# Kernel optimization log

Measured on AMD Instinct MI355X. Metric: run time of the kernel, lower is better.

Reference implementation:

```python
import jax, jax.numpy as jnp
import numpy as np

B, N_ENC, N_DEC = 32, 512, 512
IN_V, OUT_V = 2000, 2000
H, F, K, P = 256, 256, 5, 4  # P = |G| (indices < P are masked to 0 before embedding)
E_ENC, E_DEC = 128, 128


def setup_inputs() -> dict:
    key = jax.random.key(0)
    ks = jax.random.split(key, 16)
    s = lambda i, shape, scale=0.05: jax.random.normal(ks[i], shape, jnp.float32) * scale
    return dict(
        xs_idx=jax.random.randint(ks[0], (B, N_ENC), 0, IN_V),
        ys_idx=jax.random.randint(ks[1], (B, N_DEC), 0, OUT_V),
        gembed_W=s(2, (IN_V, F)),
        gconv_W=s(3, (K, F, F)),
        gdecode_W=s(4, (F, OUT_V)),
        enc_embed=s(5, (IN_V, E_ENC)),
        dec_embed=s(6, (OUT_V, E_DEC)),
        enc_Wih=s(7, (4 * H, E_ENC)),
        enc_Whh=s(8, (4 * H, H)),
        enc_b=jnp.zeros((4 * H,), jnp.float32),
        dec_Wih=s(9, (4 * H, E_DEC)),
        dec_Whh=s(10, (4 * H, H)),
        dec_b=jnp.zeros((4 * H,), jnp.float32),
        T=jax.random.uniform(ks[11], (H, 2 * H), jnp.float32, -0.5, 0.5),
    )


def _lstm(x, Wih, Whh, b, h0, c0):
    # x: (B, T, D); PyTorch gate order i, f, g, o
    def step(carry, xt):
        h, c = carry
        z = xt @ Wih.T + h @ Whh.T + b
        i, f, g, o = jnp.split(z, 4, axis=-1)
        c = jax.nn.sigmoid(f) * c + jax.nn.sigmoid(i) * jnp.tanh(g)
        h = jax.nn.sigmoid(o) * jnp.tanh(c)
        return (h, c), h
    (hT, cT), hs = jax.lax.scan(step, (h0, c0), jnp.swapaxes(x, 0, 1))
    return jnp.swapaxes(hs, 0, 1), hT, cT


def reference(xs_idx, ys_idx, gembed_W, gconv_W, gdecode_W, enc_embed, dec_embed,
              enc_Wih, enc_Whh, enc_b, dec_Wih, dec_Whh, dec_b, T):
    # --- G-equivariant stack: per-encoder-position distribution over output vocab ---
    e = jnp.tanh(gembed_W[xs_idx])  # (B, Ne, F)
    c = jax.lax.conv_general_dilated(e, gconv_W, (1,), 'SAME',
                                     dimension_numbers=('NWC', 'WIO', 'NWC'))
    probs = jax.nn.softmax(jnp.tanh(c) @ gdecode_W, axis=-1)  # (B, Ne, V)
    # encoder_scores[b, i, j] = probs[b, i, ys[b, j]]
    idx = jnp.broadcast_to(ys_idx[:, None, :], (probs.shape[0], probs.shape[1], ys_idx.shape[1]))
    encoder_scores = jnp.take_along_axis(probs, idx, axis=2)  # (B, Ne, Nd)

    # --- invariant LSTM encoder (indices < |G| masked to 0) ---
    xm = jnp.where(xs_idx < P, 0, xs_idx)
    x_embed = enc_embed[xm]  # (B, Ne, E)
    z = jnp.zeros((x_embed.shape[0], H), jnp.float32)
    henc, hT, cT = _lstm(x_embed, enc_Wih, enc_Whh, enc_b, z, z)
    hback, _, _ = _lstm(jnp.flip(x_embed, axis=1), enc_Wih, enc_Whh, enc_b, z, z)
    hback = jnp.flip(hback, axis=1)

    # --- decoder LSTM, initialized with encoder final state ---
    ym = jnp.where(ys_idx < P, 0, ys_idx)
    y_embed = dec_embed[ym]
    out, _, _ = _lstm(y_embed, dec_Wih, dec_Whh, dec_b, hT, cT)
    h_dec = jnp.concatenate([henc[:, -1:, :], out], axis=1)[:, :-1, :]  # (B, Nd, H)
    h_enc = jnp.concatenate([henc, hback], axis=2)  # (B, Ne, 2H)

    # --- bilinear alignment scores: eij[b, i, j] = h_dec[b, j] . (T @ h_enc[b, i]) ---
    Th = jnp.einsum('he,bie->bih', T, h_enc)           # (B, Ne, H)
    eij = jnp.einsum('bjh,bih->bij', h_dec, Th)        # (B, Ne, Nd)
    align = jax.nn.softmax(eij, axis=1)                # softmax over encoder positions

    p = jnp.sum(jnp.log(jnp.sum(encoder_scores * align, axis=1)), axis=1)  # (B,)
    return -jnp.sum(p)
```

## Files before the change

kernel.cpp:

```cpp
#include <hip/hip_runtime.h>

typedef _Float16 f16;
typedef _Float16 f16x2 __attribute__((ext_vector_type(2)));
typedef _Float16 f16x4 __attribute__((ext_vector_type(4)));
typedef _Float16 f16x8 __attribute__((ext_vector_type(8)));
typedef float    f32x4 __attribute__((ext_vector_type(4)));
typedef int      i32x4 __attribute__((ext_vector_type(4)));
typedef unsigned int u32;
typedef unsigned short u16;

#define DEVI static __device__ __forceinline__

static constexpr int LDT = 40;
static constexpr int LDA = 264;

DEVI float sigf(float x){ return 1.f/(1.f + __expf(-x)); }
DEVI float tanh_c(float x){
  x = fminf(fmaxf(x, -15.f), 15.f);
  float e = __expf(2.f*x);
  return (e - 1.f)/(e + 1.f);
}
DEVI float sig_f(float x){ return __builtin_amdgcn_rcpf(1.f + __expf(-x)); }
DEVI float tanh_f(float x){ return 1.f - 2.f*__builtin_amdgcn_rcpf(1.f + __expf(2.f*x)); }
DEVI float wmax16(float v){
  #pragma unroll
  for (int m=1;m<16;m<<=1) v = fmaxf(v, __shfl_xor(v, m, 64));
  return v;
}
DEVI float wsum16(float v){
  #pragma unroll
  for (int m=1;m<16;m<<=1) v += __shfl_xor(v, m, 64);
  return v;
}
DEVI f16x8 frag_ld(const f16* p){ return *(const f16x8*)p; }
DEVI void stage_tileh(int t256, const f16* src, int ld, f16* dst){
  int row = t256>>2, qq = t256&3;
  *(f16x8*)(dst + row*LDT + qq*8) = *(const f16x8*)(src + (size_t)row*ld + qq*8);
}
#define ZERO4(acc) { f32x4 _z = {0.f,0.f,0.f,0.f}; acc[0]=_z; acc[1]=_z; acc[2]=_z; acc[3]=_z; }

DEVI void gemm64h(int t256, const f16* A, int lda, const f16* Bm, int ldb, int K,
                  f16* lA, f16* lB, f32x4 acc[4]){
  const int lane = t256 & 63, wv = t256 >> 6;
  const int l15 = lane & 15, kq = lane >> 4;
  for (int k0=0; k0<K; k0+=32){
    __syncthreads();
    stage_tileh(t256, A + k0, lda, lA);
    stage_tileh(t256, Bm + k0, ldb, lB);
    __syncthreads();
    f16x8 af = frag_ld(lA + (16*wv + l15)*LDT + kq*8);
    #pragma unroll
    for (int nt=0; nt<4; nt++){
      f16x8 bf = frag_ld(lB + (16*nt + l15)*LDT + kq*8);
      acc[nt] = __builtin_amdgcn_mfma_f32_16x16x32_f16(af, bf, acc[nt], 0,0,0);
    }
  }
}

__global__ void k_cvt(const float* __restrict__ s, f16* __restrict__ d, int n){
  int i = blockIdx.x*256 + threadIdx.x;
  if (i < n) d[i] = (f16)s[i];
}
__global__ void k_gconvT(const float* __restrict__ s, f16* __restrict__ d){
  int id = blockIdx.x;
  int fo = threadIdx.x;
  d[(size_t)fo*1280 + id] = (f16)s[(size_t)id*256 + fo];
}
__global__ void k_gdecT(const float* __restrict__ s, f16* __restrict__ d){
  int v = blockIdx.x, f = threadIdx.x;
  f16 val = (f16)0.f;
  if (v < 2000) val = (f16)s[(size_t)f*2000 + v];
  d[(size_t)v*256 + f] = val;
}
__global__ void k_epad(const int* __restrict__ xs, const float* __restrict__ gemb, f16* __restrict__ epad){
  int id = blockIdx.x;
  int f = threadIdx.x;
  int b = id / 516, p = id % 516;
  float v = 0.f;
  if (p >= 2 && p < 514){ int idx = xs[b*512 + p - 2]; v = tanh_c(gemb[(size_t)idx*256 + f]); }
  epad[(size_t)id*256 + f] = (f16)v;
}
__global__ void k_embx(const int* __restrict__ xs, const int* __restrict__ ys,
                       const float* __restrict__ eemb, const float* __restrict__ demb,
                       f16* __restrict__ xo, f16* __restrict__ yo){
  int id = blockIdx.x; int f = threadIdx.x;
  bool dec = id >= 32*512; int id2 = dec ? id - 32*512 : id;
  int idx = dec ? ys[id2] : xs[id2];
  if (idx < 4) idx = 0;
  const float* src = (dec ? demb : eemb) + (size_t)idx*128;
  (dec ? yo : xo)[(size_t)id2*128 + f] = (f16)src[f];
}

__global__ void k_wmax(const float* __restrict__ Whh, u32* __restrict__ ws){
  int i = (blockIdx.x*256 + threadIdx.x)*4;
  float m = 0.f;
  #pragma unroll
  for (int j=0;j<4;j++) m = fmaxf(m, fabsf(Whh[i+j]));
  #pragma unroll
  for (int d=1; d<64; d<<=1) m = fmaxf(m, __shfl_xor(m, d, 64));
  if ((threadIdx.x & 63) == 0) atomicMax(ws, __float_as_uint(m));
}
__global__ void k_wq8(const float* __restrict__ Whh, const u32* __restrict__ ws,
                      i32x4* __restrict__ Wq){
  const int bid = blockIdx.x;
  const int l = threadIdx.x;
  const int kt = bid & 3, t8 = (bid >> 2) & 7, w = bid >> 5;
  const int r15 = l & 15;
  const int u4 = r15 >> 2, g = r15 & 3;
  const int unit = w*32 + t8*4 + u4;
  const int row = g*256 + unit;
  const int k0  = kt*64 + (l >> 4)*16;
  const float scale = 127.f / __uint_as_float(ws[0]);
  int dw[4];
  #pragma unroll
  for (int d=0; d<4; d++){
    u32 acc = 0;
    #pragma unroll
    for (int j=0; j<4; j++){
      float q = __builtin_rintf(Whh[(size_t)row*256 + k0 + d*4 + j] * scale);
      int qi = (int)fminf(fmaxf(q, -127.f), 127.f);
      acc |= ((u32)qi & 0xffu) << (8*j);
    }
    dw[d] = (int)acc;
  }
  i32x4 v = { dw[0], dw[1], dw[2], dw[3] };
  Wq[(size_t)bid*64 + l] = v;
}

__global__ __launch_bounds__(256,4) void k_conv(const f16* __restrict__ epad, const f16* __restrict__ gcT, f16* __restrict__ tf){
  __shared__ f16 lA[64*LDT], lB[64*LDT];
  const int m0 = blockIdx.x*64, n0 = blockIdx.y*64;
  const int b = m0 >> 9, n = m0 & 511;
  f32x4 acc[4]; ZERO4(acc);
  gemm64h(threadIdx.x, epad + ((size_t)b*516 + n)*256, 256, gcT + (size_t)n0*1280, 1280, 1280, lA, lB, acc);
  const int lane=threadIdx.x&63, wv=threadIdx.x>>6, l15=lane&15, kq=lane>>4;
  #pragma unroll
  for (int nt=0;nt<4;nt++)
    #pragma unroll
    for (int r=0;r<4;r++)
      tf[(size_t)(m0 + 16*wv + 4*kq + r)*256 + n0 + nt*16 + l15] = (f16)tanh_c(acc[nt][r]);
}

DEVI void ku_body(int t256, int m0, int n0, const f16* X, const f16* Wih,
                  const float* bias, f16* U, f16* lA, f16* lB){
  f32x4 acc[4]; ZERO4(acc);
  gemm64h(t256, X + (size_t)m0*128, 128, Wih + (size_t)n0*128, 128, 128, lA, lB, acc);
  const int lane=t256&63, wv=t256>>6, l15=lane&15, kq=lane>>4;
  #pragma unroll
  for (int nt=0;nt<4;nt++){
    int n = n0 + nt*16 + l15;
    float bv = bias[n];
    int cnew = (n & 255)*4 + (n >> 8);
    #pragma unroll
    for (int r=0;r<4;r++)
      U[(size_t)(m0 + 16*wv + 4*kq + r)*1024 + cnew] = (f16)(acc[nt][r] + bv);
  }
}

__global__ __launch_bounds__(256,4) void k_u(const f16* __restrict__ X, const f16* __restrict__ Wih,
                                             const float* __restrict__ bias, f16* __restrict__ U){
  __shared__ f16 lA[64*LDT], lB[64*LDT];
  ku_body(threadIdx.x, blockIdx.x*64, blockIdx.y*64, X, Wih, bias, U, lA, lB);
}

DEVI void th_body(int t256, int m0, int n0, const f16* henh, const f16* Tf, f16* Th,
                  f16* lA, f16* lB){
  f32x4 acc[4]; ZERO4(acc);
  gemm64h(t256, henh + (size_t)m0*512, 512, Tf + (size_t)n0*512, 512, 512, lA, lB, acc);
  const int lane=t256&63, wv=t256>>6, l15=lane&15, kq=lane>>4;
  #pragma unroll
  for (int nt=0;nt<4;nt++)
    #pragma unroll
    for (int r=0;r<4;r++)
      Th[(size_t)(m0 + 16*wv + 4*kq + r)*256 + n0 + nt*16 + l15] = (f16)acc[nt][r];
}

DEVI void pass1_body(int tid, int mt, int ns, const f16* tf, const f16* gdT,
                     float* mxp, float* sep, f16* lA, f16* lB2, float* mxs2, float* ses2){
  const int half = tid >> 8, t256 = tid & 255;
  const int lane = tid & 63, wv = t256 >> 6, l15 = lane & 15, kq = lane >> 4;
  f16* lB = lB2 + half*(64*LDT);
  {
    const f16* A = tf + (size_t)mt*64*256;
    int row = tid >> 3, c8 = tid & 7;
    #pragma unroll
    for (int q=0;q<4;q++)
      *(f16x8*)(lA + row*LDA + c8*32 + q*8) = *(const f16x8*)(A + (size_t)row*256 + c8*32 + q*8);
  }
  if (t256 < 64){ mxs2[half*64 + t256] = -1e30f; ses2[half*64 + t256] = 0.f; }
  __syncthreads();
  for (int nci=0; nci<4; nci++){
    const int nc = half*4 + nci;
    const int nbase = ns*512 + nc*64;
    const f16* Bm = gdT + (size_t)nbase*256;
    f32x4 acc[4]; ZERO4(acc);
    for (int k0=0; k0<256; k0+=32){
      __syncthreads();
      stage_tileh(t256, Bm + k0, 256, lB);
      __syncthreads();
      f16x8 af = frag_ld(lA + (16*wv + l15)*LDA + k0 + kq*8);
      #pragma unroll
      for (int nt=0; nt<4; nt++){
        f16x8 bf = frag_ld(lB + (16*nt + l15)*LDT + kq*8);
        acc[nt] = __builtin_amdgcn_mfma_f32_16x16x32_f16(af, bf, acc[nt], 0,0,0);
      }
    }
    #pragma unroll
    for (int r=0;r<4;r++){
      float av[4]; float cm = -1e30f;
      #pragma unroll
      for (int nt=0;nt<4;nt++){
        int gcol = nbase + nt*16 + l15;
        float a = (gcol < 2000) ? acc[nt][r] : -1e30f;
        av[nt] = a; cm = fmaxf(cm, a);
      }
      cm = wmax16(cm);
      int rr = half*64 + 16*wv + 4*kq + r;
      float old = mxs2[rr];
      float nm = fmaxf(old, cm);
      float ss = 0.f;
      #pragma unroll
      for (int nt=0;nt<4;nt++) ss += __expf(av[nt] - nm);
      ss = wsum16(ss);
      if (l15 == 0){
        ses2[rr] = ses2[rr]*__expf(old - nm) + ss;
        mxs2[rr] = nm;
      }
    }
  }
  __syncthreads();
  if (tid < 64){
    float m0 = mxs2[tid], m1 = mxs2[64+tid];
    float nm = fmaxf(m0, m1);
    float se = ses2[tid]*__expf(m0-nm) + ses2[64+tid]*__expf(m1-nm);
    mxp[(size_t)ns*16384 + mt*64 + tid] = nm;
    sep[(size_t)ns*16384 + mt*64 + tid] = se;
  }
}

__global__ void k_comb1(const float* __restrict__ mxp, const float* __restrict__ sep,
                        float* __restrict__ mx, float* __restrict__ se){
  int m = blockIdx.x*256 + threadIdx.x;
  float best = -1e30f;
  #pragma unroll
  for (int k=0;k<4;k++) best = fmaxf(best, mxp[(size_t)k*16384 + m]);
  float s = 0.f;
  #pragma unroll
  for (int k=0;k<4;k++) s += sep[(size_t)k*16384 + m] * __expf(mxp[(size_t)k*16384 + m] - best);
  mx[m] = best; se[m] = s;
}

DEVI void pass2_body(int t256, int it, int jt, int b, const f16* tf, const f16* gdT,
                     const int* ys, const float* mx, const float* se, f16* scT,
                     f16* lA, f16* lB, int* jv){
  const int lane=t256&63, wv=t256>>6, l15=lane&15, kq=lane>>4;
  if (t256<64) jv[t256] = ys[b*512 + jt*64 + t256];
  const f16* A = tf + ((size_t)b*512 + it*64)*256;
  f32x4 acc[4]; ZERO4(acc);
  for (int k0=0;k0<256;k0+=32){
    __syncthreads();
    stage_tileh(t256, A + k0, 256, lA);
    { int row=t256>>2, qq=t256&3;
      *(f16x8*)(lB + row*LDT + qq*8) = *(const f16x8*)(gdT + (size_t)jv[row]*256 + k0 + qq*8); }
    __syncthreads();
    f16x8 af = frag_ld(lA + (16*wv+l15)*LDT + kq*8);
    #pragma unroll
    for (int nt=0;nt<4;nt++){
      f16x8 bf = frag_ld(lB + (16*nt+l15)*LDT + kq*8);
      acc[nt] = __builtin_amdgcn_mfma_f32_16x16x32_f16(af, bf, acc[nt], 0,0,0);
    }
  }
  float mxv[4], rsev[4];
  #pragma unroll
  for (int r=0;r<4;r++){
    int i_ = it*64 + 16*wv + 4*kq + r;
    mxv[r] = mx[b*512 + i_];
    rsev[r] = 1.f / se[b*512 + i_];
  }
  #pragma unroll
  for (int nt=0;nt<4;nt++){
    int j_ = jt*64 + nt*16 + l15;
    #pragma unroll
    for (int r=0;r<4;r++){
      int i_ = it*64 + 16*wv + 4*kq + r;
      scT[((size_t)b*512 + j_)*512 + i_] = (f16)(__expf(acc[nt][r] - mxv[r]) * rsev[r]);
    }
  }
}

__global__ __launch_bounds__(256,2) void k_final(const f16* __restrict__ hdec, const f16* __restrict__ Th,
                                                 const f16* __restrict__ scT,
                                                 float* __restrict__ pmx, float* __restrict__ pden, float* __restrict__ pnum){
  __shared__ f16 lA[64*LDA];
  __shared__ f16 lB[64*LDT];
  __shared__ float mx_s[64], den_s[64], num_s[64];
  const int is = blockIdx.x, jt = blockIdx.y, b = blockIdx.z;
  const int tid = threadIdx.x, lane=tid&63, wv=tid>>6, l15=lane&15, kq=lane>>4;
  {
    const f16* A = hdec + ((size_t)b*512 + jt*64)*256;
    int row = tid>>2, qq = tid&3;
    #pragma unroll
    for (int c=0;c<8;c++)
      *(f16x8*)(lA + row*LDA + c*32 + qq*8) = *(const f16x8*)(A + (size_t)row*256 + c*32 + qq*8);
  }
  if (tid<64){ mx_s[tid]=-1e30f; den_s[tid]=0.f; num_s[tid]=0.f; }
  __syncthreads();
  for (int ic=0; ic<4; ic++){
    const int i0 = is*256 + ic*64;
    const f16* Bm = Th + ((size_t)b*512 + i0)*256;
    f32x4 acc[4]; ZERO4(acc);
    for (int k0=0;k0<256;k0+=32){
      __syncthreads();
      stage_tileh(tid, Bm + k0, 256, lB);
      __syncthreads();
      f16x8 af = frag_ld(lA + (16*wv+l15)*LDA + k0 + kq*8);
      #pragma unroll
      for (int nt=0;nt<4;nt++){
        f16x8 bf = frag_ld(lB + (16*nt+l15)*LDT + kq*8);
        acc[nt] = __builtin_amdgcn_mfma_f32_16x16x32_f16(af, bf, acc[nt], 0,0,0);
      }
    }
    #pragma unroll
    for (int r=0;r<4;r++){
      int jl = 16*wv + 4*kq + r;
      float av[4]; float cm=-1e30f;
      #pragma unroll
      for (int nt=0;nt<4;nt++){ av[nt]=acc[nt][r]; cm=fmaxf(cm,av[nt]); }
      cm = wmax16(cm);
      float old = mx_s[jl], nm = fmaxf(old, cm);
      float ds=0.f, nsum=0.f;
      const size_t srow = ((size_t)b*512 + jt*64 + jl)*512;
      #pragma unroll
      for (int nt=0;nt<4;nt++){
        float e = __expf(av[nt]-nm);
        float sc = (float)scT[srow + i0 + nt*16 + l15];
        ds += e; nsum += sc*e;
      }
      ds = wsum16(ds); nsum = wsum16(nsum);
      if (l15==0){
        float fac = __expf(old-nm);
        den_s[jl] = den_s[jl]*fac + ds;
        num_s[jl] = num_s[jl]*fac + nsum;
        mx_s[jl] = nm;
      }
    }
  }
  __syncthreads();
  if (tid<64){
    size_t idx = (((size_t)b*512) + jt*64 + tid)*2 + is;
    pmx[idx]=mx_s[tid]; pden[idx]=den_s[tid]; pnum[idx]=num_s[tid];
  }
}

__global__ void k_comb2(const float* __restrict__ pmx, const float* __restrict__ pden,
                        const float* __restrict__ pnum, float* __restrict__ out){
  const int b = blockIdx.x, j = threadIdx.x;
  size_t base = ((size_t)b*512 + j)*2;
  float m0=pmx[base], m1=pmx[base+1];
  float m = fmaxf(m0,m1);
  float e0=__expf(m0-m), e1=__expf(m1-m);
  float den = pden[base]*e0 + pden[base+1]*e1;
  float num = pnum[base]*e0 + pnum[base+1]*e1;
  float lp = __logf(num) - __logf(den);
  __shared__ float red[512];
  red[j] = lp;
  __syncthreads();
  for (int st=256; st>0; st>>=1){ if (j<st) red[j]+=red[j+st]; __syncthreads(); }
  if (j==0) atomicAdd(out, -red[0]);
}

DEVI void lstm_core(char* smem, const f16* U, const i32x4* Wq, const u32* ws,
                    u16* hout, float* hTcT, u16* hdec0, int nsteps, int mode, int bid)
{
  char* h8b = smem;
  const int tid = threadIdx.x;
  const int lane = tid & 63, w = tid >> 6;
  const int l15 = lane & 15, kq = lane >> 4;
  const int s = l15 & 3, p = l15 >> 2;
  const int uA = w*32 + 4*p + kq;
  const int uB = uA + 16;

  int dir = 0, b0;
  if (mode == 0){ dir = bid >> 3; b0 = (bid & 7)*4; }
  else b0 = bid*4;

  const float zscale = __uint_as_float(ws[0]) * (1.f/(127.f*127.f));

  i32x4 aw[32];
  #pragma unroll
  for (int f=0; f<32; f++) aw[f] = Wq[(size_t)(w*32 + f)*64 + lane];

  float cA = 0.f, cB = 0.f;
  if (mode == 0){
    ((u32*)h8b)[tid] = 0u;
  } else {
    const float* hp = hTcT + (size_t)(b0+s)*512;
    float hA = hp[uA], hB = hp[uB];
    cA = hp[256 + uA]; cB = hp[256 + uB];
    h8b[((uA>>4)*4 + s)*16 + (uA&15)] = (char)(int)__builtin_rintf(hA*127.f);
    h8b[((uB>>4)*4 + s)*16 + (uB&15)] = (char)(int)__builtin_rintf(hB*127.f);
  }

  const f16* Urow = U + (size_t)(b0+s)*512*1024;
  f16x4 uvA, uvB;
  {
    int tp0 = dir ? (nsteps-1) : 0;
    uvA = *(const f16x4*)(Urow + (size_t)tp0*1024 + uA*4);
    uvB = *(const f16x4*)(Urow + (size_t)tp0*1024 + uB*4);
  }
  __syncthreads();

  int cur = 0;
  #pragma unroll 1
  for (int t=0; t<nsteps; ++t){
    const int tpos = dir ? (nsteps-1-t) : t;
    int tn = dir ? (nsteps-2-t >= 0 ? nsteps-2-t : 0) : (t+1 < nsteps ? t+1 : nsteps-1);
    f16x4 puA = *(const f16x4*)(Urow + (size_t)tn*1024 + uA*4);
    f16x4 puB = *(const f16x4*)(Urow + (size_t)tn*1024 + uB*4);

    const char* hc = h8b + cur*1024;
    i32x4 bf[4];
    #pragma unroll
    for (int kt=0; kt<4; kt++)
      bf[kt] = *(const i32x4*)(hc + ((kt*4 + kq)*4 + s)*16);

    const int nxt = cur ^ 1;
    char* hn = h8b + nxt*1024;

    i32x4 acc0[4];
    #pragma unroll
    for (int t8=0; t8<4; t8++){
      i32x4 d = {0,0,0,0};
      #pragma unroll
      for (int kt=0; kt<4; kt++)
        d = __builtin_amdgcn_mfma_i32_16x16x64_i8(aw[t8*4+kt], bf[kt], d, 0,0,0);
      acc0[t8] = d;
    }

    i32x4 vA;
    #pragma unroll
    for (int e=0; e<4; e++){
      int x01 = (p&1) ? acc0[1][e] : acc0[0][e];
      int x23 = (p&1) ? acc0[3][e] : acc0[2][e];
      vA[e] = (p&2) ? x23 : x01;
    }
    float hA_;
    {
      float z0 = fmaf((float)vA[0], zscale, (float)uvA[0]);
      float z1 = fmaf((float)vA[1], zscale, (float)uvA[1]);
      float z2 = fmaf((float)vA[2], zscale, (float)uvA[2]);
      float z3 = fmaf((float)vA[3], zscale, (float)uvA[3]);
      cA = sig_f(z1)*cA + sig_f(z0)*tanh_f(z2);
      hA_ = sig_f(z3)*tanh_f(cA);
    }
    hn[((uA>>4)*4 + s)*16 + (uA&15)] = (char)(int)__builtin_rintf(hA_*127.f);

    i32x4 acc1[4];
    #pragma unroll
    for (int t8=0; t8<4; t8++){
      i32x4 d = {0,0,0,0};
      #pragma unroll
      for (int kt=0; kt<4; kt++)
        d = __builtin_amdgcn_mfma_i32_16x16x64_i8(aw[(t8+4)*4+kt], bf[kt], d, 0,0,0);
      acc1[t8] = d;
    }

    i32x4 vB;
    #pragma unroll
    for (int e=0; e<4; e++){
      int y01 = (p&1) ? acc1[1][e] : acc1[0][e];
      int y23 = (p&1) ? acc1[3][e] : acc1[2][e];
      vB[e] = (p&2) ? y23 : y01;
    }
    float hB_;
    {
      float z0 = fmaf((float)vB[0], zscale, (float)uvB[0]);
      float z1 = fmaf((float)vB[1], zscale, (float)uvB[1]);
      float z2 = fmaf((float)vB[2], zscale, (float)uvB[2]);
      float z3 = fmaf((float)vB[3], zscale, (float)uvB[3]);
      cB = sig_f(z1)*cB + sig_f(z0)*tanh_f(z2);
      hB_ = sig_f(z3)*tanh_f(cB);
    }
    hn[((uB>>4)*4 + s)*16 + (uB&15)] = (char)(int)__builtin_rintf(hB_*127.f);

    f16 fA = (f16)hA_, fB = (f16)hB_;
    if (mode == 0){
      u16* hr = hout + ((size_t)(b0+s)*512 + tpos)*512 + dir*256;
      hr[uA] = __builtin_bit_cast(u16, fA);
      hr[uB] = __builtin_bit_cast(u16, fB);
      if (!dir && t == nsteps-1){
        hdec0[(size_t)(b0+s)*512*256 + uA] = __builtin_bit_cast(u16, fA);
        hdec0[(size_t)(b0+s)*512*256 + uB] = __builtin_bit_cast(u16, fB);
        float* hp = hTcT + (size_t)(b0+s)*512;
        hp[uA] = hA_; hp[uB] = hB_;
        hp[256+uA] = cA; hp[256+uB] = cB;
      }
    } else {
      u16* hr = hout + ((size_t)(b0+s)*512 + (t+1))*256;
      hr[uA] = __builtin_bit_cast(u16, fA);
      hr[uB] = __builtin_bit_cast(u16, fB);
    }

    asm volatile("s_waitcnt lgkmcnt(0)" ::: "memory");
    __builtin_amdgcn_s_barrier();
    asm volatile("" ::: "memory");
    __builtin_amdgcn_sched_barrier(0);

    cur = nxt;
    uvA = puA; uvB = puB;
  }
}

__global__ __launch_bounds__(512,2) void k_mega_enc(
    const f16* __restrict__ Uenc, const i32x4* __restrict__ Wqe, const u32* __restrict__ wse,
    u16* __restrict__ henh, float* __restrict__ hTcT, u16* __restrict__ hdec0,
    const f16* __restrict__ tf, const f16* __restrict__ gdT,
    float* __restrict__ mxp, float* __restrict__ sep,
    const f16* __restrict__ yemb, const f16* __restrict__ Wihd,
    const float* __restrict__ db, f16* __restrict__ Udec)
{
  __shared__ __align__(16) char smem[45056];
  const int bid = blockIdx.x;
  const int tid = threadIdx.x;
  if (bid < 16){
    lstm_core(smem, Uenc, Wqe, wse, henh, hTcT, hdec0, 512, 0, bid);
    return;
  }
  if (bid >= 256 && bid < 272) return;
  const int w = (bid < 256) ? (bid - 16) : (bid - 32);
  for (int v = w; v < 3072; v += 480){
    __syncthreads();
    if (v < 1024){
      int mt = v >> 2;
      int ns = v & 3;
      pass1_body(tid, mt, ns, tf, gdT, mxp, sep,
                 (f16*)smem, (f16*)(smem + 33792), (float*)(smem + 44032), (float*)(smem + 44544));
    } else {
      int vb = v - 1024;
      int half = tid >> 8, t256 = tid & 255;
      int vbm = vb >> 4, ny = vb & 15;
      int m0 = (vbm*2 + half)*64;
      int n0 = ny*64;
      char* base = smem + half*10240;
      ku_body(t256, m0, n0, yemb, Wihd, db, Udec, (f16*)base, (f16*)(base + 5120));
    }
  }
}

__global__ __launch_bounds__(512,2) void k_mega_dec(
    const f16* __restrict__ Udec, const i32x4* __restrict__ Wqd, const u32* __restrict__ wsd,
    u16* __restrict__ hdec, float* __restrict__ hTcT,
    const f16* __restrict__ tf, const f16* __restrict__ gdT, const int* __restrict__ ys,
    const float* __restrict__ mx, const float* __restrict__ se, f16* __restrict__ scT,
    const f16* __restrict__ henh, const f16* __restrict__ Tf, f16* __restrict__ Th)
{
  __shared__ __align__(16) char smem[24576];
  const int bid = blockIdx.x;
  const int tid = threadIdx.x;
  if (bid < 8){
    lstm_core(smem, Udec, Wqd, wsd, hdec, hTcT, hdec, 511, 1, bid);
    return;
  }
  if (bid >= 256 && bid < 264) return;
  const int w = (bid < 256) ? (bid - 8) : (bid - 16);
  for (int v = w; v < 1536; v += 496){
    __syncthreads();
    if (v < 1024){
      int half = tid >> 8, t256 = tid & 255;
      int b = v >> 5, rem = v & 31;
      int jt = rem >> 2, it = (rem & 3)*2 + half;
      char* base = smem + half*10496;
      pass2_body(t256, it, jt, b, tf, gdT, ys, mx, se, scT,
                 (f16*)base, (f16*)(base + 5120), (int*)(base + 10240));
    } else {
      int vb = v - 1024;
      int half = tid >> 8, t256 = tid & 255;
      int m0 = ((vb >> 2)*2 + half)*64;
      int n0 = (vb & 3)*64;
      char* base = smem + half*10240;
      th_body(t256, m0, n0, henh, Tf, Th, (f16*)base, (f16*)(base + 5120));
    }
  }
}

extern "C" void kernel_launch(void* const* d_in, const int* in_sizes, int n_in,
                              void* d_out, int out_size, void* d_ws, size_t ws_size,
                              hipStream_t stream)
{
  (void)in_sizes; (void)n_in; (void)out_size;
  const int*   xs    = (const int*)d_in[0];
  const int*   ys    = (const int*)d_in[1];
  const float* gemb  = (const float*)d_in[2];
  const float* gconv = (const float*)d_in[3];
  const float* gdec  = (const float*)d_in[4];
  const float* eemb  = (const float*)d_in[5];
  const float* demb  = (const float*)d_in[6];
  const float* eWih  = (const float*)d_in[7];
  const float* eWhh  = (const float*)d_in[8];
  const float* eb    = (const float*)d_in[9];
  const float* dWih  = (const float*)d_in[10];
  const float* dWhh  = (const float*)d_in[11];
  const float* db    = (const float*)d_in[12];
  const float* Tm    = (const float*)d_in[13];

  char* wsb = (char*)d_ws;
  size_t off = 0;
  auto take = [&](size_t bytes)->char*{ char* p = wsb + off; off += (bytes + 255) & ~(size_t)255; return p; };
  f16* epad  = (f16*)take((size_t)32*516*256*2);
  f16* tf    = (f16*)take((size_t)32*512*256*2);
  f16* xemb  = (f16*)take((size_t)32*512*128*2);
  f16* yemb  = (f16*)take((size_t)32*512*128*2);
  f16* Uenc  = (f16*)take((size_t)32*512*1024*2);
  f16* Udec  = (f16*)take((size_t)32*512*1024*2);
  f16* henh  = (f16*)take((size_t)32*512*512*2);
  f16* hdec  = (f16*)take((size_t)32*512*256*2);
  f16* Th    = (f16*)take((size_t)32*512*256*2);
  f16* scT   = (f16*)take((size_t)32*512*512*2);
  float* mx  = (float*)take((size_t)16384*4);
  float* se  = (float*)take((size_t)16384*4);
  float* mxp = (float*)take((size_t)4*16384*4);
  float* sep = (float*)take((size_t)4*16384*4);
  float* pmx = (float*)take((size_t)32*512*2*4);
  float* pden= (float*)take((size_t)32*512*2*4);
  float* pnum= (float*)take((size_t)32*512*2*4);
  float* hTcT= (float*)take((size_t)32*512*4);
  f16* Wihe  = (f16*)take((size_t)1024*128*2);
  f16* Wihd  = (f16*)take((size_t)1024*128*2);
  f16* Tf    = (f16*)take((size_t)256*512*2);
  f16* gcT   = (f16*)take((size_t)256*1280*2);
  f16* gdT   = (f16*)take((size_t)2048*256*2);
  i32x4* Wq8e = (i32x4*)take((size_t)256*64*16);
  i32x4* Wq8d = (i32x4*)take((size_t)256*64*16);
  u32* wsc   = (u32*)take(8);
  if (off > ws_size) return;

  hipMemsetAsync(d_out, 0, sizeof(float), stream);
  hipMemsetAsync(wsc, 0, 8, stream);

  k_cvt<<<dim3(512),  256, 0, stream>>>(eWih, Wihe, 1024*128);
  k_cvt<<<dim3(512),  256, 0, stream>>>(dWih, Wihd, 1024*128);
  k_cvt<<<dim3(512),  256, 0, stream>>>(Tm,   Tf,   256*512);
  k_gconvT<<<dim3(1280), 256, 0, stream>>>(gconv, gcT);
  k_gdecT <<<dim3(2048), 256, 0, stream>>>(gdec, gdT);
  k_wmax<<<dim3(256), 256, 0, stream>>>(eWhh, wsc + 0);
  k_wmax<<<dim3(256), 256, 0, stream>>>(dWhh, wsc + 1);
  k_wq8<<<dim3(256), 64, 0, stream>>>(eWhh, wsc + 0, Wq8e);
  k_wq8<<<dim3(256), 64, 0, stream>>>(dWhh, wsc + 1, Wq8d);
  k_epad<<<dim3(32*516), 256, 0, stream>>>(xs, gemb, epad);
  k_embx<<<dim3(2*32*512), 128, 0, stream>>>(xs, ys, eemb, demb, xemb, yemb);

  k_conv<<<dim3(256,4), 256, 0, stream>>>(epad, gcT, tf);
  k_u<<<dim3(256,16), 256, 0, stream>>>(xemb, Wihe, eb, Uenc);

  k_mega_enc<<<dim3(512), 512, 0, stream>>>(Uenc, Wq8e, wsc + 0, (u16*)henh, hTcT, (u16*)hdec,
                                            tf, gdT, mxp, sep, yemb, Wihd, db, Udec);
  k_comb1<<<dim3(64), 256, 0, stream>>>(mxp, sep, mx, se);

  k_mega_dec<<<dim3(512), 512, 0, stream>>>(Udec, Wq8d, wsc + 1, (u16*)hdec, hTcT,
                                            tf, gdT, ys, mx, se, scT, henh, Tf, Th);

  k_final<<<dim3(2,8,32), 256, 0, stream>>>(hdec, Th, scT, pmx, pden, pnum);
  k_comb2<<<dim3(32), 512, 0, stream>>>(pmx, pden, pnum, (float*)d_out);
}
```

Before: 1.140 ms.

## Software-pipeline LSTM recurrence across two half-unit groups with staggered gate math

Splits the hidden units into two halves (A: units 0-127, B: 128-255) and reorders the quantized recurrent weights to match. The B-half gate nonlinearities from the previous step are interleaved with the A-half MFMAs of the current step, using explicit sched_barriers and a mid-step barrier so the second half of the K dimension is read after B's h is written. The aim is to hide transcendental and elementwise latency on the serial recurrence critical path behind matrix-core work. The cost is an extra barrier per step, a one-step-delayed B pipeline with an epilogue, and more complex indexing that is easy to get subtly wrong.

```diff
diff --git a/kernel.cpp b/kernel.cpp
--- a/kernel.cpp
+++ b/kernel.cpp
@@ -10,18 +10,16 @@
 typedef unsigned short u16;
 
 #define DEVI static __device__ __forceinline__
+#define SBAR() __builtin_amdgcn_sched_barrier(0)
 
 static constexpr int LDT = 40;
 static constexpr int LDA = 264;
 
-DEVI float sigf(float x){ return 1.f/(1.f + __expf(-x)); }
 DEVI float tanh_c(float x){
   x = fminf(fmaxf(x, -15.f), 15.f);
   float e = __expf(2.f*x);
   return (e - 1.f)/(e + 1.f);
 }
-DEVI float sig_f(float x){ return __builtin_amdgcn_rcpf(1.f + __expf(-x)); }
-DEVI float tanh_f(float x){ return 1.f - 2.f*__builtin_amdgcn_rcpf(1.f + __expf(2.f*x)); }
 DEVI float wmax16(float v){
   #pragma unroll
   for (int m=1;m<16;m<<=1) v = fmaxf(v, __shfl_xor(v, m, 64));
@@ -107,7 +105,7 @@
   const int kt = bid & 3, t8 = (bid >> 2) & 7, w = bid >> 5;
   const int r15 = l & 15;
   const int u4 = r15 >> 2, g = r15 & 3;
-  const int unit = w*32 + t8*4 + u4;
+  const int unit = (t8 < 4) ? (w*16 + t8*4 + u4) : (128 + w*16 + (t8-4)*4 + u4);
   const int row = g*256 + unit;
   const int k0  = kt*64 + (l >> 4)*16;
   const float scale = 127.f / __uint_as_float(ws[0]);
@@ -377,8 +375,9 @@
   const int lane = tid & 63, w = tid >> 6;
   const int l15 = lane & 15, kq = lane >> 4;
   const int s = l15 & 3, p = l15 >> 2;
-  const int uA = w*32 + 4*p + kq;
-  const int uB = uA + 16;
+  const int uA = w*16 + 4*p + kq;
+  const int uB = uA + 128;
+  const int u15 = uA & 15;
 
   int dir = 0, b0;
   if (mode == 0){ dir = bid >> 3; b0 = (bid & 7)*4; }
@@ -391,23 +390,31 @@
   for (int f=0; f<32; f++) aw[f] = Wq[(size_t)(w*32 + f)*64 + lane];
 
   float cA = 0.f, cB = 0.f;
+  f16 fB_init = (f16)0.f;
+  char hB_q0 = 0;
   if (mode == 0){
     ((u32*)h8b)[tid] = 0u;
   } else {
     const float* hp = hTcT + (size_t)(b0+s)*512;
-    float hA = hp[uA], hB = hp[uB];
+    float hA0 = hp[uA], hB0 = hp[uB];
     cA = hp[256 + uA]; cB = hp[256 + uB];
-    h8b[((uA>>4)*4 + s)*16 + (uA&15)] = (char)(int)__builtin_rintf(hA*127.f);
-    h8b[((uB>>4)*4 + s)*16 + (uB&15)] = (char)(int)__builtin_rintf(hB*127.f);
+    h8b[(w*4 + s)*16 + u15]     = (char)(int)__builtin_rintf(hA0*127.f);
+    hB_q0 = (char)(int)__builtin_rintf(hB0*127.f);
+    h8b[((8+w)*4 + s)*16 + u15] = hB_q0;
+    fB_init = (f16)hB0;
   }
 
   const f16* Urow = U + (size_t)(b0+s)*512*1024;
-  f16x4 uvA, uvB;
+  f16x4 uvA, uvB, uvBp;
   {
     int tp0 = dir ? (nsteps-1) : 0;
     uvA = *(const f16x4*)(Urow + (size_t)tp0*1024 + uA*4);
     uvB = *(const f16x4*)(Urow + (size_t)tp0*1024 + uB*4);
   }
+  uvBp = uvB;
+  i32x4 accBp[4];
+  { i32x4 z = {0,0,0,0}; accBp[0]=z; accBp[1]=z; accBp[2]=z; accBp[3]=z; }
+  int tpos_prev = dir ? (nsteps-1) : 0;
   __syncthreads();
 
   int cur = 0;
@@ -418,96 +425,161 @@
     f16x4 puA = *(const f16x4*)(Urow + (size_t)tn*1024 + uA*4);
     f16x4 puB = *(const f16x4*)(Urow + (size_t)tn*1024 + uB*4);
 
-    const char* hc = h8b + cur*1024;
-    i32x4 bf[4];
-    #pragma unroll
-    for (int kt=0; kt<4; kt++)
-      bf[kt] = *(const i32x4*)(hc + ((kt*4 + kq)*4 + s)*16);
-
+    char* bufc = h8b + cur*1024;
     const int nxt = cur ^ 1;
-    char* hn = h8b + nxt*1024;
-
-    i32x4 acc0[4];
-    #pragma unroll
-    for (int t8=0; t8<4; t8++){
-      i32x4 d = {0,0,0,0};
-      #pragma unroll
-      for (int kt=0; kt<4; kt++)
-        d = __builtin_amdgcn_mfma_i32_16x16x64_i8(aw[t8*4+kt], bf[kt], d, 0,0,0);
-      acc0[t8] = d;
-    }
-
-    i32x4 vA;
+    char* bufn = h8b + nxt*1024;
+    const bool live = (t > 0);
+
+    i32x4 bf0 = *(const i32x4*)(bufc + (kq*4 + s)*16);
+    i32x4 bf1 = *(const i32x4*)(bufc + ((4+kq)*4 + s)*16);
+
+    i32x4 accA[4], accB[4];
+    { i32x4 z = {0,0,0,0};
+      accA[0]=z; accA[1]=z; accA[2]=z; accA[3]=z;
+      accB[0]=z; accB[1]=z; accB[2]=z; accB[3]=z; }
+
+    i32x4 vB;
     #pragma unroll
     for (int e=0; e<4; e++){
-      int x01 = (p&1) ? acc0[1][e] : acc0[0][e];
-      int x23 = (p&1) ? acc0[3][e] : acc0[2][e];
-      vA[e] = (p&2) ? x23 : x01;
-    }
-    float hA_;
-    {
-      float z0 = fmaf((float)vA[0], zscale, (float)uvA[0]);
-      float z1 = fmaf((float)vA[1], zscale, (float)uvA[1]);
-      float z2 = fmaf((float)vA[2], zscale, (float)uvA[2]);
-      float z3 = fmaf((float)vA[3], zscale, (float)uvA[3]);
-      cA = sig_f(z1)*cA + sig_f(z0)*tanh_f(z2);
-      hA_ = sig_f(z3)*tanh_f(cA);
-    }
-    hn[((uA>>4)*4 + s)*16 + (uA&15)] = (char)(int)__builtin_rintf(hA_*127.f);
-
-    i32x4 acc1[4];
-    #pragma unroll
-    for (int t8=0; t8<4; t8++){
-      i32x4 d = {0,0,0,0};
-      #pragma unroll
-      for (int kt=0; kt<4; kt++)
-        d = __builtin_amdgcn_mfma_i32_16x16x64_i8(aw[(t8+4)*4+kt], bf[kt], d, 0,0,0);
-      acc1[t8] = d;
-    }
-
-    i32x4 vB;
-    #pragma unroll
-    for (int e=0; e<4; e++){
-      int y01 = (p&1) ? acc1[1][e] : acc1[0][e];
-      int y23 = (p&1) ? acc1[3][e] : acc1[2][e];
-      vB[e] = (p&2) ? y23 : y01;
-    }
-    float hB_;
-    {
-      float z0 = fmaf((float)vB[0], zscale, (float)uvB[0]);
-      float z1 = fmaf((float)vB[1], zscale, (float)uvB[1]);
-      float z2 = fmaf((float)vB[2], zscale, (float)uvB[2]);
-      float z3 = fmaf((float)vB[3], zscale, (float)uvB[3]);
-      cB = sig_f(z1)*cB + sig_f(z0)*tanh_f(z2);
-      hB_ = sig_f(z3)*tanh_f(cB);
-    }
-    hn[((uB>>4)*4 + s)*16 + (uB&15)] = (char)(int)__builtin_rintf(hB_*127.f);
-
-    f16 fA = (f16)hA_, fB = (f16)hB_;
+      int x01 = (p&1) ? accBp[1][e] : accBp[0][e];
+      int x23 = (p&1) ? accBp[3][e] : accBp[2][e];
+      vB[e] = (p&2) ? x23 : x01;
+    }
+    float zb0 = fmaf((float)vB[0], zscale, (float)uvBp[0]);
+    float zb1 = fmaf((float)vB[1], zscale, (float)uvBp[1]);
+    float zb2 = fmaf((float)vB[2], zscale, (float)uvBp[2]);
+    float zb3 = fmaf((float)vB[3], zscale, (float)uvBp[3]);
+    SBAR();
+    #pragma unroll
+    for (int t8=0; t8<4; t8++) accA[t8] = __builtin_amdgcn_mfma_i32_16x16x64_i8(aw[t8*4+0], bf0, accA[t8], 0,0,0);
+    SBAR();
+    float eb0 = __expf(-zb0), eb1 = __expf(-zb1), eb2 = __expf(2.f*zb2), eb3 = __expf(-zb3);
+    SBAR();
+    #pragma unroll
+    for (int t8=0; t8<4; t8++) accB[t8] = __builtin_amdgcn_mfma_i32_16x16x64_i8(aw[(4+t8)*4+0], bf0, accB[t8], 0,0,0);
+    SBAR();
+    float bi = __builtin_amdgcn_rcpf(1.f + eb0);
+    float bfg= __builtin_amdgcn_rcpf(1.f + eb1);
+    float bg = 1.f - 2.f*__builtin_amdgcn_rcpf(1.f + eb2);
+    float bo = __builtin_amdgcn_rcpf(1.f + eb3);
+    SBAR();
+    #pragma unroll
+    for (int t8=0; t8<4; t8++) accA[t8] = __builtin_amdgcn_mfma_i32_16x16x64_i8(aw[t8*4+1], bf1, accA[t8], 0,0,0);
+    SBAR();
+    float cBn = bfg*cB + bi*bg;
+    float ebc = __expf(2.f*cBn);
+    float tB  = 1.f - 2.f*__builtin_amdgcn_rcpf(1.f + ebc);
+    float hB_ = bo*tB;
+    cB = live ? cBn : cB;
+    char hq   = live ? (char)(int)__builtin_rintf(hB_*127.f) : hB_q0;
+    f16 fB    = live ? (f16)hB_ : fB_init;
+    bufc[((8+w)*4 + s)*16 + u15] = hq;
     if (mode == 0){
-      u16* hr = hout + ((size_t)(b0+s)*512 + tpos)*512 + dir*256;
-      hr[uA] = __builtin_bit_cast(u16, fA);
-      hr[uB] = __builtin_bit_cast(u16, fB);
-      if (!dir && t == nsteps-1){
-        hdec0[(size_t)(b0+s)*512*256 + uA] = __builtin_bit_cast(u16, fA);
-        hdec0[(size_t)(b0+s)*512*256 + uB] = __builtin_bit_cast(u16, fB);
-        float* hp = hTcT + (size_t)(b0+s)*512;
-        hp[uA] = hA_; hp[uB] = hB_;
-        hp[256+uA] = cA; hp[256+uB] = cB;
-      }
+      hout[(((size_t)(b0+s)*512 + tpos_prev)*512) + dir*256 + uB] = __builtin_bit_cast(u16, fB);
     } else {
-      u16* hr = hout + ((size_t)(b0+s)*512 + (t+1))*256;
-      hr[uA] = __builtin_bit_cast(u16, fA);
-      hr[uB] = __builtin_bit_cast(u16, fB);
-    }
+      hout[((size_t)(b0+s)*512 + (tpos_prev+1))*256 + uB] = __builtin_bit_cast(u16, fB);
+    }
+    SBAR();
+    #pragma unroll
+    for (int t8=0; t8<4; t8++) accB[t8] = __builtin_amdgcn_mfma_i32_16x16x64_i8(aw[(4+t8)*4+1], bf1, accB[t8], 0,0,0);
 
     asm volatile("s_waitcnt lgkmcnt(0)" ::: "memory");
     __builtin_amdgcn_s_barrier();
     asm volatile("" ::: "memory");
     __builtin_amdgcn_sched_barrier(0);
 
-    cur = nxt;
-    uvA = puA; uvB = puB;
+    i32x4 bf2 = *(const i32x4*)(bufc + ((8+kq)*4 + s)*16);
+    i32x4 bf3 = *(const i32x4*)(bufc + ((12+kq)*4 + s)*16);
+
+    #pragma unroll
+    for (int t8=0; t8<4; t8++) accA[t8] = __builtin_amdgcn_mfma_i32_16x16x64_i8(aw[t8*4+2], bf2, accA[t8], 0,0,0);
+    SBAR();
+    #pragma unroll
+    for (int t8=0; t8<4; t8++) accA[t8] = __builtin_amdgcn_mfma_i32_16x16x64_i8(aw[t8*4+3], bf3, accA[t8], 0,0,0);
+    SBAR();
+    i32x4 vA;
+    #pragma unroll
+    for (int e=0; e<4; e++){
+      int x01 = (p&1) ? accA[1][e] : accA[0][e];
+      int x23 = (p&1) ? accA[3][e] : accA[2][e];
+      vA[e] = (p&2) ? x23 : x01;
+    }
+    float za0 = fmaf((float)vA[0], zscale, (float)uvA[0]);
+    float za1 = fmaf((float)vA[1], zscale, (float)uvA[1]);
+    float za2 = fmaf((float)vA[2], zscale, (float)uvA[2]);
+    float za3 = fmaf((float)vA[3], zscale, (float)uvA[3]);
+    SBAR();
+    #pragma unroll
+    for (int t8=0; t8<4; t8++) accB[t8] = __builtin_amdgcn_mfma_i32_16x16x64_i8(aw[(4+t8)*4+2], bf2, accB[t8], 0,0,0);
+    SBAR();
+    float ea0 = __expf(-za0), ea1 = __expf(-za1), ea2 = __expf(2.f*za2), ea3 = __expf(-za3);
+    SBAR();
+    #pragma unroll
+    for (int t8=0; t8<4; t8++) accB[t8] = __builtin_amdgcn_mfma_i32_16x16x64_i8(aw[(4+t8)*4+3], bf3, accB[t8], 0,0,0);
+    SBAR();
+    float ai = __builtin_amdgcn_rcpf(1.f + ea0);
+    float af = __builtin_amdgcn_rcpf(1.f + ea1);
+    float ag = 1.f - 2.f*__builtin_amdgcn_rcpf(1.f + ea2);
+    float ao = __builtin_amdgcn_rcpf(1.f + ea3);
+    cA = af*cA + ai*ag;
+    float eac = __expf(2.f*cA);
+    float tA  = 1.f - 2.f*__builtin_amdgcn_rcpf(1.f + eac);
+    float hA_ = ao*tA;
+    bufn[(w*4 + s)*16 + u15] = (char)(int)__builtin_rintf(hA_*127.f);
+    f16 fA = (f16)hA_;
+    if (mode == 0){
+      hout[(((size_t)(b0+s)*512 + tpos)*512) + dir*256 + uA] = __builtin_bit_cast(u16, fA);
+      if (!dir && t == nsteps-1){
+        hdec0[(size_t)(b0+s)*512*256 + uA] = __builtin_bit_cast(u16, fA);
+        float* hp = hTcT + (size_t)(b0+s)*512;
+        hp[uA] = hA_; hp[256+uA] = cA;
+      }
+    } else {
+      hout[((size_t)(b0+s)*512 + (t+1))*256 + uA] = __builtin_bit_cast(u16, fA);
+    }
+
+    asm volatile("s_waitcnt lgkmcnt(0)" ::: "memory");
+    __builtin_amdgcn_s_barrier();
+    asm volatile("" ::: "memory");
+    __builtin_amdgcn_sched_barrier(0);
+
+    accBp[0]=accB[0]; accBp[1]=accB[1]; accBp[2]=accB[2]; accBp[3]=accB[3];
+    uvBp = uvB; uvA = puA; uvB = puB;
+    tpos_prev = tpos; cur = nxt;
+  }
+
+  {
+    i32x4 vB;
+    #pragma unroll
+    for (int e=0; e<4; e++){
+      int x01 = (p&1) ? accBp[1][e] : accBp[0][e];
+      int x23 = (p&1) ? accBp[3][e] : accBp[2][e];
+      vB[e] = (p&2) ? x23 : x01;
+    }
+    float zb0 = fmaf((float)vB[0], zscale, (float)uvBp[0]);
+    float zb1 = fmaf((float)vB[1], zscale, (float)uvBp[1]);
+    float zb2 = fmaf((float)vB[2], zscale, (float)uvBp[2]);
+    float zb3 = fmaf((float)vB[3], zscale, (float)uvBp[3]);
+    float eb0 = __expf(-zb0), eb1 = __expf(-zb1), eb2 = __expf(2.f*zb2), eb3 = __expf(-zb3);
+    float bi = __builtin_amdgcn_rcpf(1.f + eb0);
+    float bfg= __builtin_amdgcn_rcpf(1.f + eb1);
+    float bg = 1.f - 2.f*__builtin_amdgcn_rcpf(1.f + eb2);
+    float bo = __builtin_amdgcn_rcpf(1.f + eb3);
+    cB = bfg*cB + bi*bg;
+    float ebc = __expf(2.f*cB);
+    float tB  = 1.f - 2.f*__builtin_amdgcn_rcpf(1.f + ebc);
+    float hB_ = bo*tB;
+    f16 fB = (f16)hB_;
+    if (mode == 0){
+      hout[(((size_t)(b0+s)*512 + tpos_prev)*512) + dir*256 + uB] = __builtin_bit_cast(u16, fB);
+      if (!dir){
+        hdec0[(size_t)(b0+s)*512*256 + uB] = __builtin_bit_cast(u16, fB);
+        float* hp = hTcT + (size_t)(b0+s)*512;
+        hp[uB] = hB_; hp[256+uB] = cB;
+      }
+    } else {
+      hout[((size_t)(b0+s)*512 + (tpos_prev+1))*256 + uB] = __builtin_bit_cast(u16, fB);
+    }
   }
 }
 
```

New measurement: 1.183 ms. 3.7% more time.
